# Kernel optimization log

Measured on AMD Instinct MI355X. Metric: run time of the kernel, lower is better.

The kernel has to match this reference:

```python
import jax, jax.numpy as jnp
import numpy as np

N = 50000
D_IN = 1024          # BioGPT hidden size
HID = 256            # gnn_hidden_dim
H1, H2 = 4, 1        # heads per layer
NEG_SLOPE = 0.2      # PyG GATv2 default


def _glorot(key, shape):
    fan_in, fan_out = shape[0], shape[-1]
    lim = (6.0 / (fan_in + fan_out)) ** 0.5
    return jax.random.uniform(key, shape, jnp.float32, -lim, lim)


def setup_inputs() -> dict:
    key = jax.random.key(0)
    ks = jax.random.split(key, 12)
    node_features = jax.random.normal(ks[0], (N, D_IN), jnp.float32)
    edge_index = jax.random.randint(ks[1], (2, 400000), 0, N, jnp.int64)
    return {
        "node_features": node_features,
        "edge_index": edge_index,
        # layer 1: GATv2Conv(1024 -> 256, heads=4)
        "W1_l": _glorot(ks[2], (D_IN, H1 * HID)),
        "b1_l": jnp.zeros((H1 * HID,), jnp.float32),
        "W1_r": _glorot(ks[3], (D_IN, H1 * HID)),
        "b1_r": jnp.zeros((H1 * HID,), jnp.float32),
        "att1": _glorot(ks[4], (H1, HID)),
        "bias1": jnp.zeros((H1 * HID,), jnp.float32),
        # layer 2: GATv2Conv(1024 -> 256, heads=1)
        "W2_l": _glorot(ks[5], (H1 * HID, H2 * HID)),
        "b2_l": jnp.zeros((H2 * HID,), jnp.float32),
        "W2_r": _glorot(ks[6], (H1 * HID, H2 * HID)),
        "b2_r": jnp.zeros((H2 * HID,), jnp.float32),
        "att2": _glorot(ks[7], (H2, HID)),
        "bias2": jnp.zeros((H2 * HID,), jnp.float32),
    }


def _gatv2(x, src, dst, Wl, bl, Wr, br, att, bias, heads):
    n = x.shape[0]
    xl = (x @ Wl + bl).reshape(n, heads, HID)  # source-side transform
    xr = (x @ Wr + br).reshape(n, heads, HID)  # target-side transform
    msg = xl[src] + xr[dst]                    # [E, H, C]
    e = jnp.where(msg > 0, msg, NEG_SLOPE * msg)
    alpha = jnp.einsum('ehc,hc->eh', e, att)   # attention logits
    amax = jax.ops.segment_max(alpha, dst, num_segments=n)
    ex = jnp.exp(alpha - amax[dst])
    denom = jax.ops.segment_sum(ex, dst, num_segments=n)
    a = ex / (denom[dst] + 1e-16)              # segment softmax per dst node
    out = jax.ops.segment_sum(a[:, :, None] * xl[src], dst, num_segments=n)
    return out.reshape(n, heads * HID) + bias


def reference(node_features, edge_index, W1_l, b1_l, W1_r, b1_r, att1, bias1,
              W2_l, b2_l, W2_r, b2_r, att2, bias2):
    n = node_features.shape[0]
    loops = jnp.arange(n, dtype=edge_index.dtype)
    src = jnp.concatenate([edge_index[0], loops])  # add self-loops (PyG default)
    dst = jnp.concatenate([edge_index[1], loops])
    x = _gatv2(node_features, src, dst, W1_l, b1_l, W1_r, b1_r, att1, bias1, H1)
    x = jax.nn.relu(x)
    # dropout(p=0.1) is identity in eval mode
    x = _gatv2(x, src, dst, W2_l, b2_l, W2_r, b2_r, att2, bias2, H2)
    return jax.nn.relu(x)
```

## Files before the change

### kernel.cpp

```cpp
#include <hip/hip_runtime.h>
#include <stdint.h>

#define D_IN 1024
#define C1   1024
#define C2   256
#define NEG  0.2f

typedef unsigned int u32;
typedef uint16_t u16;
typedef __attribute__((ext_vector_type(8))) short bf16x8;
typedef __attribute__((ext_vector_type(4))) float f32x4;

__device__ __forceinline__ float bf2f(u32 lo16) { return __uint_as_float(lo16 << 16); }
__device__ __forceinline__ u16 f2bf(float f) {
  u32 u = __float_as_uint(f);
  u += 0x7fffu + ((u >> 16) & 1u);
  return (u16)(u >> 16);
}

__device__ __forceinline__ void gload16(const u16* g, u16* l) {
  __builtin_amdgcn_global_load_lds(
      (const __attribute__((address_space(1))) unsigned int*)g,
      (__attribute__((address_space(3))) unsigned int*)l,
      16, 0, 0);
}

__global__ void cast_x_k(const float* __restrict__ x, u16* __restrict__ A,
                         int nrows, int Mp) {
  long long idx = (long long)blockIdx.x * blockDim.x + threadIdx.x;
  long long total = (long long)Mp * (D_IN / 8);
  if (idx >= total) return;
  long long base = idx * 8;
  int row = (int)(base >> 10);
  u32 o0 = 0, o1 = 0, o2 = 0, o3 = 0;
  if (row < nrows) {
    const float4* px = (const float4*)(x + base);
    float4 v0 = px[0], v1 = px[1];
    o0 = (u32)f2bf(v0.x) | ((u32)f2bf(v0.y) << 16);
    o1 = (u32)f2bf(v0.z) | ((u32)f2bf(v0.w) << 16);
    o2 = (u32)f2bf(v1.x) | ((u32)f2bf(v1.y) << 16);
    o3 = (u32)f2bf(v1.z) | ((u32)f2bf(v1.w) << 16);
  }
  *(uint4*)(A + base) = make_uint4(o0, o1, o2, o3);
}

__global__ void transpose_cast_k(const float* __restrict__ W, u16* __restrict__ Wt,
                                 int K, int Nc) {
  __shared__ float sh[32][33];
  int k0 = blockIdx.x * 32, n0 = blockIdx.y * 32;
  int tx = threadIdx.x, ty = threadIdx.y;
#pragma unroll
  for (int i = 0; i < 32; i += 8)
    sh[ty + i][tx] = W[(long long)(k0 + ty + i) * Nc + (n0 + tx)];
  __syncthreads();
#pragma unroll
  for (int i = 0; i < 32; i += 8)
    Wt[(long long)(n0 + ty + i) * K + (k0 + tx)] = f2bf(sh[tx][ty + i]);
}

__global__ void concat_bias_k(const float* __restrict__ a, const float* __restrict__ b,
                              float* __restrict__ o, int na, int nb) {
  int i = blockIdx.x * 256 + threadIdx.x;
  if (i < na) o[i] = a[i];
  else if (i < na + nb) o[i] = b[i - na];
}

template <int TN>
__global__ __launch_bounds__(512, 2) void gemm8_k(
    const u16* __restrict__ A, const u16* __restrict__ Bt,
    const float* __restrict__ bias, u16* __restrict__ C, int K) {
  __shared__ u16 As[2][2][8192];
  __shared__ u16 Bs[2][2][8192];
  const int nx = gridDim.x, ny = gridDim.y;
  const int nwg = nx * ny;
  int id = blockIdx.y * nx + blockIdx.x;
  int q = nwg >> 3, r = nwg & 7;
  int xcd = id & 7, loc = id >> 3;
  int sid = (xcd < r ? xcd * (q + 1) : r * (q + 1) + (xcd - r) * q) + loc;
  const int m0 = (sid / ny) * 256;
  const int n0 = (sid % ny) * 256;

  const int tid = threadIdx.x;
  const int lane = tid & 63;
  const int wave = tid >> 6;
  const int wm = wave >> 2;
  const int wn = wave & 3;
  const int bh = wn >> 1;
  const int bql = (wn & 1) * 2048;

  const int srow = tid >> 2;
  const int kq   = tid & 3;
  const int ksw  = (kq ^ ((srow >> 1) & 3)) * 8;

  const int nt = K / 64;

  const u16* gA[2] = { A + (long long)(m0 + srow) * K + ksw,
                       A + (long long)(m0 + 128 + srow) * K + ksw };
  const u16* gB[2] = { Bt + (long long)(n0 + srow) * K + ksw,
                       Bt + (long long)(n0 + 128 + srow) * K + ksw };

  auto stageA = [&](int kt, int h) {
    int db = kt & 1;
    gload16(gA[h] + kt * 64,      &As[db][h][tid * 8]);
    gload16(gA[h] + kt * 64 + 32, &As[db][h][4096 + tid * 8]);
  };
  auto stageB = [&](int kt, int h) {
    int db = kt & 1;
    gload16(gB[h] + kt * 64,      &Bs[db][h][tid * 8]);
    gload16(gB[h] + kt * 64 + 32, &Bs[db][h][4096 + tid * 8]);
  };

  const int rbase = (lane & 15) * 32 + (((lane >> 4) ^ ((lane >> 1) & 3)) << 3);

  f32x4 acc[8][4] = {};
  bf16x8 av[4][2], bv[4][2];

  stageA(0, 0); stageA(0, 1); stageB(0, 0); stageB(0, 1);
  if (nt > 1) {
    stageA(1, 0);
    asm volatile("s_waitcnt vmcnt(2)" ::: "memory");
  } else {
    asm volatile("s_waitcnt vmcnt(0)" ::: "memory");
  }
  __builtin_amdgcn_s_barrier();

  for (int t = 0; t < nt; ++t) {
    const int cur = t & 1;
    const u16* Al = &As[cur][wm][0];
    const u16* Bl = &Bs[cur][bh][0];

    if (t + 1 < nt) { stageB(t + 1, 0); stageB(t + 1, 1); }
#pragma unroll
    for (int i = 0; i < 4; ++i) {
      av[i][0] = *(const bf16x8*)(Al + i * 512 + rbase);
      av[i][1] = *(const bf16x8*)(Al + 4096 + i * 512 + rbase);
    }
#pragma unroll
    for (int j = 0; j < 2; ++j) {
      bv[j][0] = *(const bf16x8*)(Bl + bql + j * 512 + rbase);
      bv[j][1] = *(const bf16x8*)(Bl + 4096 + bql + j * 512 + rbase);
    }
    __builtin_amdgcn_s_barrier();
    __builtin_amdgcn_s_setprio(1);
#pragma unroll
    for (int i = 0; i < 4; ++i)
#pragma unroll
      for (int j = 0; j < 2; ++j) {
        acc[i][j] = __builtin_amdgcn_mfma_f32_16x16x32_bf16(av[i][0], bv[j][0], acc[i][j], 0, 0, 0);
        acc[i][j] = __builtin_amdgcn_mfma_f32_16x16x32_bf16(av[i][1], bv[j][1], acc[i][j], 0, 0, 0);
      }
    __builtin_amdgcn_s_setprio(0);
    __builtin_amdgcn_s_barrier();

    if (t + 1 < nt) stageA(t + 1, 1);
#pragma unroll
    for (int j = 2; j < 4; ++j) {
      bv[j][0] = *(const bf16x8*)(Bl + bql + j * 512 + rbase);
      bv[j][1] = *(const bf16x8*)(Bl + 4096 + bql + j * 512 + rbase);
    }
    __builtin_amdgcn_s_barrier();
    __builtin_amdgcn_s_setprio(1);
#pragma unroll
    for (int i = 0; i < 4; ++i)
#pragma unroll
      for (int j = 2; j < 4; ++j) {
        acc[i][j] = __builtin_amdgcn_mfma_f32_16x16x32_bf16(av[i][0], bv[j][0], acc[i][j], 0, 0, 0);
        acc[i][j] = __builtin_amdgcn_mfma_f32_16x16x32_bf16(av[i][1], bv[j][1], acc[i][j], 0, 0, 0);
      }
    __builtin_amdgcn_s_setprio(0);
    __builtin_amdgcn_s_barrier();

#pragma unroll
    for (int i = 0; i < 4; ++i) {
      av[i][0] = *(const bf16x8*)(Al + (4 + i) * 512 + rbase);
      av[i][1] = *(const bf16x8*)(Al + 4096 + (4 + i) * 512 + rbase);
    }
    __builtin_amdgcn_s_barrier();
    __builtin_amdgcn_s_setprio(1);
#pragma unroll
    for (int i = 0; i < 4; ++i)
#pragma unroll
      for (int j = 2; j < 4; ++j) {
        acc[4 + i][j] = __builtin_amdgcn_mfma_f32_16x16x32_bf16(av[i][0], bv[j][0], acc[4 + i][j], 0, 0, 0);
        acc[4 + i][j] = __builtin_amdgcn_mfma_f32_16x16x32_bf16(av[i][1], bv[j][1], acc[4 + i][j], 0, 0, 0);
      }
    __builtin_amdgcn_s_setprio(0);
    __builtin_amdgcn_s_barrier();

    if (t + 2 < nt) stageA(t + 2, 0);
    __builtin_amdgcn_s_barrier();
    __builtin_amdgcn_s_setprio(1);
#pragma unroll
    for (int i = 0; i < 4; ++i)
#pragma unroll
      for (int j = 0; j < 2; ++j) {
        acc[4 + i][j] = __builtin_amdgcn_mfma_f32_16x16x32_bf16(av[i][0], bv[j][0], acc[4 + i][j], 0, 0, 0);
        acc[4 + i][j] = __builtin_amdgcn_mfma_f32_16x16x32_bf16(av[i][1], bv[j][1], acc[4 + i][j], 0, 0, 0);
      }
    __builtin_amdgcn_s_setprio(0);
    if (t + 2 < nt) {
      asm volatile("s_waitcnt vmcnt(2)" ::: "memory");
    } else if (t + 1 < nt) {
      asm volatile("s_waitcnt vmcnt(0)" ::: "memory");
    }
    __builtin_amdgcn_s_barrier();
  }

#pragma unroll
  for (int mf = 0; mf < 8; ++mf) {
    int r0 = m0 + wm * 128 + mf * 16 + ((lane >> 4) << 2);
#pragma unroll
    for (int nf = 0; nf < 4; ++nf) {
      int c = n0 + wn * 64 + nf * 16 + (lane & 15);
      float b = bias[c];
#pragma unroll
      for (int j = 0; j < 4; ++j)
        C[(long long)(r0 + j) * TN + c] = f2bf(acc[mf][nf][j] + b);
    }
  }
}

__global__ void count_k(const int* __restrict__ ei, int* __restrict__ counts,
                        int E0, int E) {
  for (int e = blockIdx.x * blockDim.x + threadIdx.x; e < E;
       e += gridDim.x * blockDim.x) {
    int dst = (e < E0) ? ei[E0 + e] : e - E0;
    atomicAdd(&counts[dst], 1);
  }
}

__global__ void blocksum_k(const int* __restrict__ counts, int* __restrict__ bsum, int n) {
  int i = blockIdx.x * 256 + threadIdx.x;
  int v = (i < n) ? counts[i] : 0;
#pragma unroll
  for (int off = 1; off < 64; off <<= 1) v += __shfl_xor(v, off);
  __shared__ int sh[4];
  if ((threadIdx.x & 63) == 0) sh[threadIdx.x >> 6] = v;
  __syncthreads();
  if (threadIdx.x == 0) bsum[blockIdx.x] = sh[0] + sh[1] + sh[2] + sh[3];
}

__global__ void scanb_k(const int* __restrict__ bsum, int* __restrict__ boff,
                        int nb, int* __restrict__ indptr, int n, int E) {
  __shared__ int sh[256];
  int i = threadIdx.x;
  int v = (i < nb) ? bsum[i] : 0;
  sh[i] = v;
  __syncthreads();
  int sum = v;
  for (int off = 1; off < 256; off <<= 1) {
    int t = (i >= off) ? sh[i - off] : 0;
    __syncthreads();
    sum += t;
    sh[i] = sum;
    __syncthreads();
  }
  if (i < nb) boff[i] = sum - v;
  if (i == 0) indptr[n] = E;
}

__global__ void scanf_k(const int* __restrict__ counts, const int* __restrict__ boff,
                        int* __restrict__ indptr, int n) {
  __shared__ int sh[256];
  int b = blockIdx.x;
  int i = b * 256 + threadIdx.x;
  int v = (i < n) ? counts[i] : 0;
  sh[threadIdx.x] = v;
  __syncthreads();
  int sum = v;
  for (int off = 1; off < 256; off <<= 1) {
    int t = (threadIdx.x >= off) ? sh[threadIdx.x - off] : 0;
    __syncthreads();
    sum += t;
    sh[threadIdx.x] = sum;
    __syncthreads();
  }
  if (i < n) indptr[i] = boff[b] + sum - v;
}

__global__ void scatter_k(const int* __restrict__ ei, const int* __restrict__ indptr,
                          int* __restrict__ cursor, int* __restrict__ esrc,
                          int E0, int E) {
  for (int e = blockIdx.x * blockDim.x + threadIdx.x; e < E;
       e += gridDim.x * blockDim.x) {
    int dst, src;
    if (e < E0) { src = ei[e]; dst = ei[E0 + e]; } else { src = dst = e - E0; }
    int pos = atomicAdd(&cursor[dst], 1);
    esrc[indptr[dst] + pos] = src;
  }
}

__global__ __launch_bounds__(256) void fused_edge1_k(
    const u16* __restrict__ XLR, const int* __restrict__ indptr,
    const int* __restrict__ esrc, const float* __restrict__ att,
    const float* __restrict__ bias, u16* __restrict__ X2, int N) {
  int d = blockIdx.x;
  int tid = threadIdx.x;
  int c0 = tid * 4;
  if (d >= N) {
    *(ushort4*)(X2 + (long long)d * C1 + c0) = make_ushort4(0, 0, 0, 0);
    return;
  }
  ushort4 xr4 = *(const ushort4*)(XLR + (long long)d * 2048 + 1024 + c0);
  float xr0 = bf2f(xr4.x), xr1 = bf2f(xr4.y), xr2 = bf2f(xr4.z), xr3 = bf2f(xr4.w);
  float4 at = *(const float4*)(att + c0);

  float m = -INFINITY, l = 0.f;
  float a0 = 0.f, a1 = 0.f, a2 = 0.f, a3 = 0.f;
  int p = indptr[d], pend = indptr[d + 1];
  int src = esrc[p];
  ushort4 xl4 = *(const ushort4*)(XLR + (long long)src * 2048 + c0);
  while (p < pend) {
    ushort4 cur = xl4;
    int pn = p + 1;
    if (pn < pend) {
      int sn = esrc[pn];
      xl4 = *(const ushort4*)(XLR + (long long)sn * 2048 + c0);
    }
    float x0 = bf2f(cur.x), x1 = bf2f(cur.y), x2 = bf2f(cur.z), x3 = bf2f(cur.w);
    float m0 = x0 + xr0, m1 = x1 + xr1, m2 = x2 + xr2, m3 = x3 + xr3;
    float e0 = m0 > 0.f ? m0 : NEG * m0;
    float e1 = m1 > 0.f ? m1 : NEG * m1;
    float e2 = m2 > 0.f ? m2 : NEG * m2;
    float e3 = m3 > 0.f ? m3 : NEG * m3;
    float s = at.x * e0 + at.y * e1 + at.z * e2 + at.w * e3;
#pragma unroll
    for (int off = 1; off < 64; off <<= 1) s += __shfl_xor(s, off);
    float mnew = fmaxf(m, s);
    float scale = __expf(m - mnew);
    float w = __expf(s - mnew);
    l = l * scale + w;
    a0 = a0 * scale + w * x0;
    a1 = a1 * scale + w * x1;
    a2 = a2 * scale + w * x2;
    a3 = a3 * scale + w * x3;
    m = mnew;
    p = pn;
  }
  float inv = 1.f / (l + 1e-16f);
  float4 b = *(const float4*)(bias + c0);
  ushort4 o;
  o.x = f2bf(fmaxf(a0 * inv + b.x, 0.f));
  o.y = f2bf(fmaxf(a1 * inv + b.y, 0.f));
  o.z = f2bf(fmaxf(a2 * inv + b.z, 0.f));
  o.w = f2bf(fmaxf(a3 * inv + b.w, 0.f));
  *(ushort4*)(X2 + (long long)d * C1 + c0) = o;
}

__global__ __launch_bounds__(256) void fused_edge2_k(
    const u16* __restrict__ XLR, const int* __restrict__ indptr,
    const int* __restrict__ esrc, const float* __restrict__ att,
    const float* __restrict__ bias, float* __restrict__ out, int N) {
  int d = blockIdx.x * 4 + (threadIdx.x >> 6);
  if (d >= N) return;
  int lane = threadIdx.x & 63;
  int c0 = lane * 4;
  ushort4 xr4 = *(const ushort4*)(XLR + (long long)d * 512 + 256 + c0);
  float xr0 = bf2f(xr4.x), xr1 = bf2f(xr4.y), xr2 = bf2f(xr4.z), xr3 = bf2f(xr4.w);
  float4 at = *(const float4*)(att + c0);

  float m = -INFINITY, l = 0.f;
  float a0 = 0.f, a1 = 0.f, a2 = 0.f, a3 = 0.f;
  int p = indptr[d], pend = indptr[d + 1];
  int src = esrc[p];
  ushort4 xl4 = *(const ushort4*)(XLR + (long long)src * 512 + c0);
  while (p < pend) {
    ushort4 cur = xl4;
    int pn = p + 1;
    if (pn < pend) {
      int sn = esrc[pn];
      xl4 = *(const ushort4*)(XLR + (long long)sn * 512 + c0);
    }
    float x0 = bf2f(cur.x), x1 = bf2f(cur.y), x2 = bf2f(cur.z), x3 = bf2f(cur.w);
    float m0 = x0 + xr0, m1 = x1 + xr1, m2 = x2 + xr2, m3 = x3 + xr3;
    float e0 = m0 > 0.f ? m0 : NEG * m0;
    float e1 = m1 > 0.f ? m1 : NEG * m1;
    float e2 = m2 > 0.f ? m2 : NEG * m2;
    float e3 = m3 > 0.f ? m3 : NEG * m3;
    float s = at.x * e0 + at.y * e1 + at.z * e2 + at.w * e3;
#pragma unroll
    for (int off = 1; off < 64; off <<= 1) s += __shfl_xor(s, off);
    float mnew = fmaxf(m, s);
    float scale = __expf(m - mnew);
    float w = __expf(s - mnew);
    l = l * scale + w;
    a0 = a0 * scale + w * x0;
    a1 = a1 * scale + w * x1;
    a2 = a2 * scale + w * x2;
    a3 = a3 * scale + w * x3;
    m = mnew;
    p = pn;
  }
  float inv = 1.f / (l + 1e-16f);
  float4 b = *(const float4*)(bias + c0);
  float4 o;
  o.x = fmaxf(a0 * inv + b.x, 0.f);
  o.y = fmaxf(a1 * inv + b.y, 0.f);
  o.z = fmaxf(a2 * inv + b.z, 0.f);
  o.w = fmaxf(a3 * inv + b.w, 0.f);
  *(float4*)(out + (long long)d * C2 + c0) = o;
}

extern "C" void kernel_launch(void* const* d_in, const int* in_sizes, int n_in,
                              void* d_out, int out_size, void* d_ws, size_t ws_size,
                              hipStream_t stream) {
  const float* x     = (const float*)d_in[0];
  const int*   ei    = (const int*)d_in[1];
  const float* W1l   = (const float*)d_in[2];
  const float* b1l   = (const float*)d_in[3];
  const float* W1r   = (const float*)d_in[4];
  const float* b1r   = (const float*)d_in[5];
  const float* att1  = (const float*)d_in[6];
  const float* bias1 = (const float*)d_in[7];
  const float* W2l   = (const float*)d_in[8];
  const float* b2l   = (const float*)d_in[9];
  const float* W2r   = (const float*)d_in[10];
  const float* b2r   = (const float*)d_in[11];
  const float* att2  = (const float*)d_in[12];
  const float* bias2 = (const float*)d_in[13];

  const int N  = in_sizes[0] / D_IN;
  const int E0 = in_sizes[1] / 2;
  const int E  = E0 + N;
  const int Mp = (N + 255) & ~255;
  const int NB = (N + 255) / 256;

  char* p = (char*)d_ws;
  auto alloc = [&](size_t bytes) -> char* {
    char* r = p;
    p += (bytes + 255) & ~(size_t)255;
    return r;
  };
  u16* A_bf  = (u16*)alloc((size_t)Mp * D_IN * 2);
  u16* XLR1  = (u16*)alloc((size_t)Mp * 2048 * 2);
  u16* W1t   = (u16*)alloc((size_t)2048 * D_IN * 2);
  u16* W2t   = (u16*)alloc((size_t)512 * C1 * 2);
  float* bc1 = (float*)alloc(2048 * 4);
  float* bc2 = (float*)alloc(512 * 4);
  int* counts = (int*)alloc((size_t)N * 4);
  int* cursor = (int*)alloc((size_t)N * 4);
  int* indptr = (int*)alloc((size_t)(N + 1) * 4);
  int* esrc   = (int*)alloc((size_t)E * 4);
  int* bsum   = (int*)alloc((size_t)NB * 4);
  int* boff   = (int*)alloc((size_t)NB * 4);
  u16* X2   = A_bf;
  u16* XLR2 = XLR1;

  size_t need = (size_t)(p - (char*)d_ws);
  if (ws_size < need) {
    hipMemsetAsync(d_out, 0xFF, 4, stream);
    return;
  }

  hipMemsetAsync(counts, 0, (size_t)N * 4, stream);
  hipMemsetAsync(cursor, 0, (size_t)N * 4, stream);

  {
    long long tot = (long long)Mp * (D_IN / 8);
    cast_x_k<<<(int)((tot + 255) / 256), 256, 0, stream>>>(x, A_bf, N, Mp);
  }
  dim3 tb(32, 8);
  transpose_cast_k<<<dim3(D_IN / 32, C1 / 32), tb, 0, stream>>>(W1l, W1t, D_IN, C1);
  transpose_cast_k<<<dim3(D_IN / 32, C1 / 32), tb, 0, stream>>>(W1r, W1t + (size_t)1024 * D_IN, D_IN, C1);
  transpose_cast_k<<<dim3(C1 / 32, C2 / 32), tb, 0, stream>>>(W2l, W2t, C1, C2);
  transpose_cast_k<<<dim3(C1 / 32, C2 / 32), tb, 0, stream>>>(W2r, W2t + (size_t)256 * C1, C1, C2);
  concat_bias_k<<<8, 256, 0, stream>>>(b1l, b1r, bc1, 1024, 1024);
  concat_bias_k<<<2, 256, 0, stream>>>(b2l, b2r, bc2, 256, 256);

  count_k<<<1024, 256, 0, stream>>>(ei, counts, E0, E);
  blocksum_k<<<NB, 256, 0, stream>>>(counts, bsum, N);
  scanb_k<<<1, 256, 0, stream>>>(bsum, boff, NB, indptr, N, E);
  scanf_k<<<NB, 256, 0, stream>>>(counts, boff, indptr, N);
  scatter_k<<<1024, 256, 0, stream>>>(ei, indptr, cursor, esrc, E0, E);

  gemm8_k<2048><<<dim3(Mp / 256, 2048 / 256), 512, 0, stream>>>(A_bf, W1t, bc1, XLR1, D_IN);
  fused_edge1_k<<<Mp, 256, 0, stream>>>(XLR1, indptr, esrc, att1, bias1, X2, N);

  gemm8_k<512><<<dim3(Mp / 256, 512 / 256), 512, 0, stream>>>(X2, W2t, bc2, XLR2, C1);
  fused_edge2_k<<<(N + 3) / 4, 256, 0, stream>>>(XLR2, indptr, esrc, att2, bias2,
                                                 (float*)d_out, N);
}
```

Before: 773.7 us.

## Reorder GEMM prefetch stages and deepen edge gather pipeline with pairwise processing

```diff
diff --git a/kernel.cpp b/kernel.cpp
--- a/kernel.cpp
+++ b/kernel.cpp
@@ -117,8 +117,8 @@
 
   stageA(0, 0); stageA(0, 1); stageB(0, 0); stageB(0, 1);
   if (nt > 1) {
-    stageA(1, 0);
-    asm volatile("s_waitcnt vmcnt(2)" ::: "memory");
+    stageB(1, 0); stageB(1, 1);
+    asm volatile("s_waitcnt vmcnt(4)" ::: "memory");
   } else {
     asm volatile("s_waitcnt vmcnt(0)" ::: "memory");
   }
@@ -129,7 +129,7 @@
     const u16* Al = &As[cur][wm][0];
     const u16* Bl = &Bs[cur][bh][0];
 
-    if (t + 1 < nt) { stageB(t + 1, 0); stageB(t + 1, 1); }
+    if (t + 1 < nt) stageA(t + 1, 0);
 #pragma unroll
     for (int i = 0; i < 4; ++i) {
       av[i][0] = *(const bf16x8*)(Al + i * 512 + rbase);
@@ -170,6 +170,7 @@
     __builtin_amdgcn_s_setprio(0);
     __builtin_amdgcn_s_barrier();
 
+    if (t + 2 < nt) stageB(t + 2, 0);
 #pragma unroll
     for (int i = 0; i < 4; ++i) {
       av[i][0] = *(const bf16x8*)(Al + (4 + i) * 512 + rbase);
@@ -187,7 +188,7 @@
     __builtin_amdgcn_s_setprio(0);
     __builtin_amdgcn_s_barrier();
 
-    if (t + 2 < nt) stageA(t + 2, 0);
+    if (t + 2 < nt) stageB(t + 2, 1);
     __builtin_amdgcn_s_barrier();
     __builtin_amdgcn_s_setprio(1);
 #pragma unroll
@@ -199,7 +200,7 @@
       }
     __builtin_amdgcn_s_setprio(0);
     if (t + 2 < nt) {
-      asm volatile("s_waitcnt vmcnt(2)" ::: "memory");
+      asm volatile("s_waitcnt vmcnt(4)" ::: "memory");
     } else if (t + 1 < nt) {
       asm volatile("s_waitcnt vmcnt(0)" ::: "memory");
     }
@@ -308,35 +309,62 @@
   float m = -INFINITY, l = 0.f;
   float a0 = 0.f, a1 = 0.f, a2 = 0.f, a3 = 0.f;
   int p = indptr[d], pend = indptr[d + 1];
-  int src = esrc[p];
-  ushort4 xl4 = *(const ushort4*)(XLR + (long long)src * 2048 + c0);
-  while (p < pend) {
-    ushort4 cur = xl4;
-    int pn = p + 1;
-    if (pn < pend) {
-      int sn = esrc[pn];
-      xl4 = *(const ushort4*)(XLR + (long long)sn * 2048 + c0);
-    }
-    float x0 = bf2f(cur.x), x1 = bf2f(cur.y), x2 = bf2f(cur.z), x3 = bf2f(cur.w);
-    float m0 = x0 + xr0, m1 = x1 + xr1, m2 = x2 + xr2, m3 = x3 + xr3;
-    float e0 = m0 > 0.f ? m0 : NEG * m0;
-    float e1 = m1 > 0.f ? m1 : NEG * m1;
-    float e2 = m2 > 0.f ? m2 : NEG * m2;
-    float e3 = m3 > 0.f ? m3 : NEG * m3;
-    float s = at.x * e0 + at.y * e1 + at.z * e2 + at.w * e3;
-#pragma unroll
-    for (int off = 1; off < 64; off <<= 1) s += __shfl_xor(s, off);
-    float mnew = fmaxf(m, s);
+  ushort4 z4 = make_ushort4(0, 0, 0, 0);
+#define LD1(ix) (*(const ushort4*)(XLR + (long long)esrc[ix] * 2048 + c0))
+  ushort4 qa = (p < pend) ? LD1(p) : z4;
+  ushort4 qb = (p + 1 < pend) ? LD1(p + 1) : z4;
+  ushort4 ra = (p + 2 < pend) ? LD1(p + 2) : z4;
+  ushort4 rb = (p + 3 < pend) ? LD1(p + 3) : z4;
+  int i = p;
+  for (; i + 1 < pend; i += 2) {
+    ushort4 ca = qa, cb = qb;
+    qa = ra; qb = rb;
+    ra = (i + 4 < pend) ? LD1(i + 4) : z4;
+    rb = (i + 5 < pend) ? LD1(i + 5) : z4;
+    float xa0 = bf2f(ca.x), xa1 = bf2f(ca.y), xa2 = bf2f(ca.z), xa3 = bf2f(ca.w);
+    float xb0 = bf2f(cb.x), xb1 = bf2f(cb.y), xb2 = bf2f(cb.z), xb3 = bf2f(cb.w);
+    float ta0 = xa0 + xr0, ta1 = xa1 + xr1, ta2 = xa2 + xr2, ta3 = xa3 + xr3;
+    float tb0 = xb0 + xr0, tb1 = xb1 + xr1, tb2 = xb2 + xr2, tb3 = xb3 + xr3;
+    ta0 = ta0 > 0.f ? ta0 : NEG * ta0;  ta1 = ta1 > 0.f ? ta1 : NEG * ta1;
+    ta2 = ta2 > 0.f ? ta2 : NEG * ta2;  ta3 = ta3 > 0.f ? ta3 : NEG * ta3;
+    tb0 = tb0 > 0.f ? tb0 : NEG * tb0;  tb1 = tb1 > 0.f ? tb1 : NEG * tb1;
+    tb2 = tb2 > 0.f ? tb2 : NEG * tb2;  tb3 = tb3 > 0.f ? tb3 : NEG * tb3;
+    float sa = at.x * ta0 + at.y * ta1 + at.z * ta2 + at.w * ta3;
+    float sb = at.x * tb0 + at.y * tb1 + at.z * tb2 + at.w * tb3;
+#pragma unroll
+    for (int off = 1; off < 64; off <<= 1) {
+      sa += __shfl_xor(sa, off);
+      sb += __shfl_xor(sb, off);
+    }
+    float mnew = fmaxf(fmaxf(m, sa), sb);
     float scale = __expf(m - mnew);
-    float w = __expf(s - mnew);
-    l = l * scale + w;
-    a0 = a0 * scale + w * x0;
-    a1 = a1 * scale + w * x1;
-    a2 = a2 * scale + w * x2;
-    a3 = a3 * scale + w * x3;
+    float wa = __expf(sa - mnew);
+    float wb = __expf(sb - mnew);
+    l = l * scale + wa + wb;
+    a0 = a0 * scale + wa * xa0 + wb * xb0;
+    a1 = a1 * scale + wa * xa1 + wb * xb1;
+    a2 = a2 * scale + wa * xa2 + wb * xb2;
+    a3 = a3 * scale + wa * xa3 + wb * xb3;
     m = mnew;
-    p = pn;
-  }
+  }
+  if (i < pend) {
+    float xa0 = bf2f(qa.x), xa1 = bf2f(qa.y), xa2 = bf2f(qa.z), xa3 = bf2f(qa.w);
+    float ta0 = xa0 + xr0, ta1 = xa1 + xr1, ta2 = xa2 + xr2, ta3 = xa3 + xr3;
+    ta0 = ta0 > 0.f ? ta0 : NEG * ta0;  ta1 = ta1 > 0.f ? ta1 : NEG * ta1;
+    ta2 = ta2 > 0.f ? ta2 : NEG * ta2;  ta3 = ta3 > 0.f ? ta3 : NEG * ta3;
+    float sa = at.x * ta0 + at.y * ta1 + at.z * ta2 + at.w * ta3;
+#pragma unroll
+    for (int off = 1; off < 64; off <<= 1) sa += __shfl_xor(sa, off);
+    float mnew = fmaxf(m, sa);
+    float scale = __expf(m - mnew);
+    float wa = __expf(sa - mnew);
+    l = l * scale + wa;
+    a0 = a0 * scale + wa * xa0;
+    a1 = a1 * scale + wa * xa1;
+    a2 = a2 * scale + wa * xa2;
+    a3 = a3 * scale + wa * xa3;
+  }
+#undef LD1
   float inv = 1.f / (l + 1e-16f);
   float4 b = *(const float4*)(bias + c0);
   ushort4 o;
@@ -362,35 +390,62 @@
   float m = -INFINITY, l = 0.f;
   float a0 = 0.f, a1 = 0.f, a2 = 0.f, a3 = 0.f;
   int p = indptr[d], pend = indptr[d + 1];
-  int src = esrc[p];
-  ushort4 xl4 = *(const ushort4*)(XLR + (long long)src * 512 + c0);
-  while (p < pend) {
-    ushort4 cur = xl4;
-    int pn = p + 1;
-    if (pn < pend) {
-      int sn = esrc[pn];
-      xl4 = *(const ushort4*)(XLR + (long long)sn * 512 + c0);
-    }
-    float x0 = bf2f(cur.x), x1 = bf2f(cur.y), x2 = bf2f(cur.z), x3 = bf2f(cur.w);
-    float m0 = x0 + xr0, m1 = x1 + xr1, m2 = x2 + xr2, m3 = x3 + xr3;
-    float e0 = m0 > 0.f ? m0 : NEG * m0;
-    float e1 = m1 > 0.f ? m1 : NEG * m1;
-    float e2 = m2 > 0.f ? m2 : NEG * m2;
-    float e3 = m3 > 0.f ? m3 : NEG * m3;
-    float s = at.x * e0 + at.y * e1 + at.z * e2 + at.w * e3;
-#pragma unroll
-    for (int off = 1; off < 64; off <<= 1) s += __shfl_xor(s, off);
-    float mnew = fmaxf(m, s);
+  ushort4 z4 = make_ushort4(0, 0, 0, 0);
+#define LD2(ix) (*(const ushort4*)(XLR + (long long)esrc[ix] * 512 + c0))
+  ushort4 qa = (p < pend) ? LD2(p) : z4;
+  ushort4 qb = (p + 1 < pend) ? LD2(p + 1) : z4;
+  ushort4 ra = (p + 2 < pend) ? LD2(p + 2) : z4;
+  ushort4 rb = (p + 3 < pend) ? LD2(p + 3) : z4;
+  int i = p;
+  for (; i + 1 < pend; i += 2) {
+    ushort4 ca = qa, cb = qb;
+    qa = ra; qb = rb;
+    ra = (i + 4 < pend) ? LD2(i + 4) : z4;
+    rb = (i + 5 < pend) ? LD2(i + 5) : z4;
+    float xa0 = bf2f(ca.x), xa1 = bf2f(ca.y), xa2 = bf2f(ca.z), xa3 = bf2f(ca.w);
+    float xb0 = bf2f(cb.x), xb1 = bf2f(cb.y), xb2 = bf2f(cb.z), xb3 = bf2f(cb.w);
+    float ta0 = xa0 + xr0, ta1 = xa1 + xr1, ta2 = xa2 + xr2, ta3 = xa3 + xr3;
+    float tb0 = xb0 + xr0, tb1 = xb1 + xr1, tb2 = xb2 + xr2, tb3 = xb3 + xr3;
+    ta0 = ta0 > 0.f ? ta0 : NEG * ta0;  ta1 = ta1 > 0.f ? ta1 : NEG * ta1;
+    ta2 = ta2 > 0.f ? ta2 : NEG * ta2;  ta3 = ta3 > 0.f ? ta3 : NEG * ta3;
+    tb0 = tb0 > 0.f ? tb0 : NEG * tb0;  tb1 = tb1 > 0.f ? tb1 : NEG * tb1;
+    tb2 = tb2 > 0.f ? tb2 : NEG * tb2;  tb3 = tb3 > 0.f ? tb3 : NEG * tb3;
+    float sa = at.x * ta0 + at.y * ta1 + at.z * ta2 + at.w * ta3;
+    float sb = at.x * tb0 + at.y * tb1 + at.z * tb2 + at.w * tb3;
+#pragma unroll
+    for (int off = 1; off < 64; off <<= 1) {
+      sa += __shfl_xor(sa, off);
+      sb += __shfl_xor(sb, off);
+    }
+    float mnew = fmaxf(fmaxf(m, sa), sb);
     float scale = __expf(m - mnew);
-    float w = __expf(s - mnew);
-    l = l * scale + w;
-    a0 = a0 * scale + w * x0;
-    a1 = a1 * scale + w * x1;
-    a2 = a2 * scale + w * x2;
-    a3 = a3 * scale + w * x3;
+    float wa = __expf(sa - mnew);
+    float wb = __expf(sb - mnew);
+    l = l * scale + wa + wb;
+    a0 = a0 * scale + wa * xa0 + wb * xb0;
+    a1 = a1 * scale + wa * xa1 + wb * xb1;
+    a2 = a2 * scale + wa * xa2 + wb * xb2;
+    a3 = a3 * scale + wa * xa3 + wb * xb3;
     m = mnew;
-    p = pn;
-  }
+  }
+  if (i < pend) {
+    float xa0 = bf2f(qa.x), xa1 = bf2f(qa.y), xa2 = bf2f(qa.z), xa3 = bf2f(qa.w);
+    float ta0 = xa0 + xr0, ta1 = xa1 + xr1, ta2 = xa2 + xr2, ta3 = xa3 + xr3;
+    ta0 = ta0 > 0.f ? ta0 : NEG * ta0;  ta1 = ta1 > 0.f ? ta1 : NEG * ta1;
+    ta2 = ta2 > 0.f ? ta2 : NEG * ta2;  ta3 = ta3 > 0.f ? ta3 : NEG * ta3;
+    float sa = at.x * ta0 + at.y * ta1 + at.z * ta2 + at.w * ta3;
+#pragma unroll
+    for (int off = 1; off < 64; off <<= 1) sa += __shfl_xor(sa, off);
+    float mnew = fmaxf(m, sa);
+    float scale = __expf(m - mnew);
+    float wa = __expf(sa - mnew);
+    l = l * scale + wa;
+    a0 = a0 * scale + wa * xa0;
+    a1 = a1 * scale + wa * xa1;
+    a2 = a2 * scale + wa * xa2;
+    a3 = a3 * scale + wa * xa3;
+  }
+#undef LD2
   float inv = 1.f / (l + 1e-16f);
   float4 b = *(const float4*)(bias + c0);
   float4 o;
```

New measurement: 783.0 us. About the same (+1.2%).
